# Kernel optimization log

Hardware: AMD Instinct MI355X
Metric: run time of the kernel (lower is better)

## Reference

```python
import jax, jax.numpy as jnp
import numpy as np

N = 8192        # total mesh nodes
M1 = 6000       # nodes set from x (full 3D coords)
M2 = 2000       # nodes set from y (coords 0 and 2 only)
B = 4           # batch
K = 4           # smoothing steps


def setup_inputs() -> dict:
    key = jax.random.key(0)
    k1, k2, k3, k4 = jax.random.split(key, 4)
    # Sparse-ish random symmetric-flavored adjacency, stored dense (as the module does).
    A = (jax.random.uniform(k1, (N, N)) < 0.002).astype(jnp.float32)
    idx = jnp.arange(N)
    # Ring edges guarantee every row has degree >= 1 (avoid divide-by-zero).
    A = A.at[idx, (idx + 1) % N].set(1.0)
    A = A.at[(idx + 1) % N, idx].set(1.0)
    # Diagonal: 1 for first half, 0 for second half -> output mask selects N//2 nodes.
    A = A.at[idx, idx].set((idx < N // 2).astype(jnp.float32))
    # Disjoint index sets for the scatter writes.
    perm = jax.random.permutation(k2, N)
    li1 = perm[:M1].astype(jnp.int64)
    li2 = perm[M1:M1 + M2].astype(jnp.int64)
    x = jax.random.normal(k3, (B, M1 * 3), dtype=jnp.float32)
    y = jax.random.normal(k4, (B, M2 * 2), dtype=jnp.float32)
    temp_zero = jnp.zeros((N, 3), dtype=jnp.float32)
    return {"x": x, "y": y, "edge_matrix": A, "temp_zero": temp_zero,
            "local_indices_1": li1, "local_indices_2": li2, "k": K}


def reference(x, y, edge_matrix, temp_zero, local_indices_1, local_indices_2, k):
    b = x.shape[0]
    # Scatter-build the graph state [B, N, 3].
    temp = jnp.broadcast_to(temp_zero[None], (b,) + temp_zero.shape)
    temp = temp.at[:, local_indices_1, :].set(x.reshape(b, -1, 3))
    y2 = y.reshape(b, -1, 2)
    temp = temp.at[:, local_indices_2, 0].set(y2[:, :, 0])
    temp = temp.at[:, local_indices_2, 2].set(y2[:, :, 1])
    # Degree normalization vector (row sums), computed once.
    deg = jnp.sum(edge_matrix, axis=1)  # [N]
    mesh = temp
    for _ in range(k):
        # smoother: (mesh^T @ A^T)^T == A @ mesh over the node dim, then /degree.
        mesh = jnp.einsum('ij,bjc->bic', edge_matrix, mesh) / deg[None, :, None]
    # Gather rows whose diagonal adjacency entry is zero.
    mask = jnp.diag(edge_matrix) == 0
    return mesh[:, mask, :]
```

## Files before the change

### kernel.cpp

```cpp
#include <hip/hip_runtime.h>

#define NN   8192
#define NN3  (NN * 3)
#define ST   16
#define CAP  64
#define M1   6000
#define M2   2000
#define SENT NN
#define CT   256
#define SB   64
#define NPS  (NN / SB)

typedef unsigned short u16;
typedef float f4v __attribute__((ext_vector_type(4)));

__global__ __launch_bounds__(256) void build_ell(const float* __restrict__ A,
                                                 u16* __restrict__ cols,
                                                 int* __restrict__ nch,
                                                 float* __restrict__ rdeg,
                                                 const int* __restrict__ li1,
                                                 const int* __restrict__ li2,
                                                 const float* __restrict__ x,
                                                 const float* __restrict__ y,
                                                 float* __restrict__ mesh_a,
                                                 float* __restrict__ mesh_b,
                                                 int B) {
    const int tid = threadIdx.x;
    __shared__ u16 enc16[NN];
    __shared__ int cnt;

    if (blockIdx.x >= NN) {
        const int sid = blockIdx.x - NN;
        for (int i = tid; i < NN; i += 256) enc16[i] = 0;
        __syncthreads();
        for (int j = tid; j < M1; j += 256) enc16[li1[j]] = (u16)(1 + j);
        for (int j = tid; j < M2; j += 256) enc16[li2[j]] = (u16)(M1 + 1 + j);
        __syncthreads();
        if (sid == 0 && tid < ST) {
            mesh_a[NN * ST + tid] = 0.f;
            mesh_b[NN * ST + tid] = 0.f;
        }
        const int lo = sid * NPS;
        for (int t = tid; t < NPS * ST; t += 256) {
            const int il = t >> 4, q = t & 15;
            const int i = lo + il;
            float v = 0.f;
            if (q < 12) {
                const u16 e = enc16[i];
                if (e) {
                    const int b = q / 3, c = q - b * 3;
                    if (e <= M1)      v = x[(b * M1 + (e - 1)) * 3 + c];
                    else if (c != 1)  v = y[(b * M2 + (e - (M1 + 1))) * 2 + (c >> 1)];
                }
            }
            mesh_a[(size_t)i * ST + q] = v;
        }
        return;
    }

    const int row = blockIdx.x;
    if (tid == 0) cnt = 0;
    __syncthreads();
    const f4v* __restrict__ Arow = (const f4v*)(A + (size_t)row * NN);
    f4v v[8];
    #pragma unroll
    for (int k = 0; k < 8; ++k)
        v[k] = __builtin_nontemporal_load(&Arow[k * 256 + tid]);
    u16* __restrict__ crow = cols + row * CAP;
    #pragma unroll
    for (int k = 0; k < 8; ++k) {
        const int base = (k * 256 + tid) * 4;
        if (v[k].x != 0.f) { int p = atomicAdd(&cnt, 1); if (p < CAP) crow[p] = (u16)(base);     }
        if (v[k].y != 0.f) { int p = atomicAdd(&cnt, 1); if (p < CAP) crow[p] = (u16)(base + 1); }
        if (v[k].z != 0.f) { int p = atomicAdd(&cnt, 1); if (p < CAP) crow[p] = (u16)(base + 2); }
        if (v[k].w != 0.f) { int p = atomicAdd(&cnt, 1); if (p < CAP) crow[p] = (u16)(base + 3); }
    }
    __syncthreads();
    int c = cnt;
    if (c > CAP) c = CAP;
    const int padded = (c + 7) & ~7;
    if (tid < padded - c && c + tid < CAP) crow[c + tid] = (u16)SENT;
    if (tid == 0) {
        nch[row]  = padded >> 3;
        rdeg[row] = 1.0f / (float)cnt;
    }
}

#define GATHER8(mb)                                                             \
    { const uint4 q = cr[ch];                                                   \
      acc += mb[(q.x & 0xFFFF) * ST + bc] + mb[(q.x >> 16) * ST + bc]           \
           + mb[(q.y & 0xFFFF) * ST + bc] + mb[(q.y >> 16) * ST + bc]           \
           + mb[(q.z & 0xFFFF) * ST + bc] + mb[(q.z >> 16) * ST + bc]           \
           + mb[(q.w & 0xFFFF) * ST + bc] + mb[(q.w >> 16) * ST + bc]; }

__global__ __launch_bounds__(CT) void spmv_full(const u16* __restrict__ cols,
                                                const int* __restrict__ nch,
                                                const float* __restrict__ rdeg,
                                                const float* __restrict__ src,
                                                float* __restrict__ dst) {
    const int g = blockIdx.x * CT + threadIdx.x;
    const int i = g / 12, bc = g - (g / 12) * 12;
    const int n = nch[i];
    const float rd = rdeg[i];
    const uint4* __restrict__ cr = (const uint4*)(cols + i * CAP);
    const float* __restrict__ mb = src;
    float acc = 0.f;
    for (int ch = 0; ch < n; ++ch) GATHER8(mb);
    dst[(size_t)i * ST + bc] = acc * rd;
}

__global__ __launch_bounds__(CT) void spmv_last(const u16* __restrict__ cols,
                                                const int* __restrict__ nch,
                                                const float* __restrict__ rdeg,
                                                const float* __restrict__ src,
                                                float* __restrict__ out) {
    const int g = blockIdx.x * CT + threadIdx.x;
    const int i2 = g / 12, bc = g - (g / 12) * 12;
    const int b = bc / 3, c = bc - b * 3;
    const int i = NN / 2 + i2;
    const int n = nch[i];
    const float rd = rdeg[i];
    const uint4* __restrict__ cr = (const uint4*)(cols + i * CAP);
    const float* __restrict__ mb = src;
    float acc = 0.f;
    for (int ch = 0; ch < n; ++ch) GATHER8(mb);
    out[((size_t)b * (NN / 2) + i2) * 3 + c] = acc * rd;
}

extern "C" void kernel_launch(void* const* d_in, const int* in_sizes, int n_in,
                              void* d_out, int out_size, void* d_ws, size_t ws_size,
                              hipStream_t stream) {
    const float* x   = (const float*)d_in[0];
    const float* y   = (const float*)d_in[1];
    const float* A   = (const float*)d_in[2];
    const int*   li1 = (const int*)d_in[4];
    const int*   li2 = (const int*)d_in[5];

    const int B = in_sizes[0] / (M1 * 3);

    char* ws = (char*)d_ws;
    u16*   cols   = (u16*)ws;    ws += (size_t)NN * CAP * 2;
    int*   nchv   = (int*)ws;    ws += (size_t)NN * 4;
    float* rdeg   = (float*)ws;  ws += (size_t)NN * 4;
    float* mesh_a = (float*)ws;  ws += (size_t)(NN + 1) * ST * 4;
    float* mesh_b = (float*)ws;

    build_ell<<<NN + SB, 256, 0, stream>>>(A, cols, nchv, rdeg,
                                           li1, li2, x, y, mesh_a, mesh_b, B);

    const int nbf = NN * 12 / CT;
    spmv_full<<<nbf, CT, 0, stream>>>(cols, nchv, rdeg, mesh_a, mesh_b);
    spmv_full<<<nbf, CT, 0, stream>>>(cols, nchv, rdeg, mesh_b, mesh_a);
    spmv_full<<<nbf, CT, 0, stream>>>(cols, nchv, rdeg, mesh_a, mesh_b);

    const int nbl = (NN / 2) * 12 / CT;
    spmv_last<<<nbl, CT, 0, stream>>>(cols, nchv, rdeg, mesh_b, (float*)d_out);
}
```

Before: 63.55 us.

## Fuse first smoothing step into ELL build kernel, drop one SpMV launch

Each row block now builds the scatter index table in shared memory and computes the first smoothing step directly from its nonzero columns, writing the normalized result into mesh_a. This removes one full SpMV kernel launch and the separate mesh initialization blocks. In exchange, every one of the row blocks redundantly rebuilds the node-index table, reading the index arrays and doing thousands of shared-memory scatters per block.

```diff
diff --git a/kernel.cpp b/kernel.cpp
--- a/kernel.cpp
+++ b/kernel.cpp
@@ -1,88 +1,86 @@
 #include <hip/hip_runtime.h>
 
 #define NN   8192
-#define NN3  (NN * 3)
 #define ST   16
 #define CAP  64
 #define M1   6000
 #define M2   2000
 #define SENT NN
 #define CT   256
-#define SB   64
-#define NPS  (NN / SB)
 
 typedef unsigned short u16;
 typedef float f4v __attribute__((ext_vector_type(4)));
 
-__global__ __launch_bounds__(256) void build_ell(const float* __restrict__ A,
-                                                 u16* __restrict__ cols,
-                                                 int* __restrict__ nch,
-                                                 float* __restrict__ rdeg,
-                                                 const int* __restrict__ li1,
-                                                 const int* __restrict__ li2,
-                                                 const float* __restrict__ x,
-                                                 const float* __restrict__ y,
-                                                 float* __restrict__ mesh_a,
-                                                 float* __restrict__ mesh_b,
-                                                 int B) {
+__global__ __launch_bounds__(256) void build_fused(
+    const float* __restrict__ A,
+    u16* __restrict__ cols, int* __restrict__ nch, float* __restrict__ rdeg,
+    const int* __restrict__ li1, const int* __restrict__ li2,
+    const float* __restrict__ x, const float* __restrict__ y,
+    float* __restrict__ mesh_a, float* __restrict__ mesh_b)
+{
+    const int row = blockIdx.x;
     const int tid = threadIdx.x;
-    __shared__ u16 enc16[NN];
-    __shared__ int cnt;
+    __shared__ u16  enc16[NN];
+    __shared__ u16  scol[CAP];
+    __shared__ float sacc[12];
+    __shared__ int  cnt;
 
-    if (blockIdx.x >= NN) {
-        const int sid = blockIdx.x - NN;
-        for (int i = tid; i < NN; i += 256) enc16[i] = 0;
-        __syncthreads();
-        for (int j = tid; j < M1; j += 256) enc16[li1[j]] = (u16)(1 + j);
-        for (int j = tid; j < M2; j += 256) enc16[li2[j]] = (u16)(M1 + 1 + j);
-        __syncthreads();
-        if (sid == 0 && tid < ST) {
-            mesh_a[NN * ST + tid] = 0.f;
-            mesh_b[NN * ST + tid] = 0.f;
-        }
-        const int lo = sid * NPS;
-        for (int t = tid; t < NPS * ST; t += 256) {
-            const int il = t >> 4, q = t & 15;
-            const int i = lo + il;
-            float v = 0.f;
-            if (q < 12) {
-                const u16 e = enc16[i];
-                if (e) {
-                    const int b = q / 3, c = q - b * 3;
-                    if (e <= M1)      v = x[(b * M1 + (e - 1)) * 3 + c];
-                    else if (c != 1)  v = y[(b * M2 + (e - (M1 + 1))) * 2 + (c >> 1)];
-                }
-            }
-            mesh_a[(size_t)i * ST + q] = v;
-        }
-        return;
-    }
-
-    const int row = blockIdx.x;
-    if (tid == 0) cnt = 0;
-    __syncthreads();
     const f4v* __restrict__ Arow = (const f4v*)(A + (size_t)row * NN);
     f4v v[8];
     #pragma unroll
     for (int k = 0; k < 8; ++k)
         v[k] = __builtin_nontemporal_load(&Arow[k * 256 + tid]);
+
+    {
+        unsigned int* e32 = (unsigned int*)enc16;
+        #pragma unroll
+        for (int t = 0; t < 16; ++t) e32[t * 256 + tid] = 0u;
+    }
+    if (tid < 12) sacc[tid] = 0.f;
+    if (tid == 0) cnt = 0;
+    __syncthreads();
+    for (int j = tid; j < M1; j += 256) enc16[li1[j]] = (u16)(1 + j);
+    for (int j = tid; j < M2; j += 256) enc16[li2[j]] = (u16)(M1 + 1 + j);
+    __syncthreads();
+
     u16* __restrict__ crow = cols + row * CAP;
     #pragma unroll
     for (int k = 0; k < 8; ++k) {
         const int base = (k * 256 + tid) * 4;
-        if (v[k].x != 0.f) { int p = atomicAdd(&cnt, 1); if (p < CAP) crow[p] = (u16)(base);     }
-        if (v[k].y != 0.f) { int p = atomicAdd(&cnt, 1); if (p < CAP) crow[p] = (u16)(base + 1); }
-        if (v[k].z != 0.f) { int p = atomicAdd(&cnt, 1); if (p < CAP) crow[p] = (u16)(base + 2); }
-        if (v[k].w != 0.f) { int p = atomicAdd(&cnt, 1); if (p < CAP) crow[p] = (u16)(base + 3); }
+        #pragma unroll
+        for (int e4 = 0; e4 < 4; ++e4) {
+            if (v[k][e4] != 0.f) {
+                const int col = base + e4;
+                const int p = atomicAdd(&cnt, 1);
+                if (p < CAP) { crow[p] = (u16)col; scol[p] = (u16)col; }
+            }
+        }
     }
     __syncthreads();
-    int c = cnt;
-    if (c > CAP) c = CAP;
-    const int padded = (c + 7) & ~7;
-    if (tid < padded - c && c + tid < CAP) crow[c + tid] = (u16)SENT;
-    if (tid == 0) {
-        nch[row]  = padded >> 3;
-        rdeg[row] = 1.0f / (float)cnt;
+
+    const int cc = (cnt > CAP) ? CAP : cnt;
+    for (int t = tid; t < cc * 12; t += 256) {
+        const int nz = t / 12, q = t - nz * 12;
+        const u16 e = enc16[scol[nz]];
+        float val = 0.f;
+        if (e) {
+            const int b = q / 3, c = q - b * 3;
+            if (e <= (u16)M1)  val = x[(b * M1 + (e - 1)) * 3 + c];
+            else if (c != 1)   val = y[(b * M2 + (e - (M1 + 1))) * 2 + (c >> 1)];
+        }
+        if (val != 0.f) atomicAdd(&sacc[q], val);
+    }
+
+    const int padded = (cc + 7) & ~7;
+    if (tid < padded - cc && cc + tid < CAP) crow[cc + tid] = (u16)SENT;
+    __syncthreads();
+
+    const float rd = 1.0f / (float)cnt;
+    if (tid == 0) { nch[row] = padded >> 3; rdeg[row] = rd; }
+    if (tid < 12) mesh_a[(size_t)row * ST + tid] = sacc[tid] * rd;
+    if (row == 0 && tid >= 32 && tid < 48) {
+        mesh_a[(size_t)NN * ST + (tid - 32)] = 0.f;
+        mesh_b[(size_t)NN * ST + (tid - 32)] = 0.f;
     }
 }
 
@@ -136,8 +134,6 @@
     const int*   li1 = (const int*)d_in[4];
     const int*   li2 = (const int*)d_in[5];
 
-    const int B = in_sizes[0] / (M1 * 3);
-
     char* ws = (char*)d_ws;
     u16*   cols   = (u16*)ws;    ws += (size_t)NN * CAP * 2;
     int*   nchv   = (int*)ws;    ws += (size_t)NN * 4;
@@ -145,14 +141,13 @@
     float* mesh_a = (float*)ws;  ws += (size_t)(NN + 1) * ST * 4;
     float* mesh_b = (float*)ws;
 
-    build_ell<<<NN + SB, 256, 0, stream>>>(A, cols, nchv, rdeg,
-                                           li1, li2, x, y, mesh_a, mesh_b, B);
+    build_fused<<<NN, 256, 0, stream>>>(A, cols, nchv, rdeg,
+                                        li1, li2, x, y, mesh_a, mesh_b);
 
     const int nbf = NN * 12 / CT;
     spmv_full<<<nbf, CT, 0, stream>>>(cols, nchv, rdeg, mesh_a, mesh_b);
     spmv_full<<<nbf, CT, 0, stream>>>(cols, nchv, rdeg, mesh_b, mesh_a);
-    spmv_full<<<nbf, CT, 0, stream>>>(cols, nchv, rdeg, mesh_a, mesh_b);
 
     const int nbl = (NN / 2) * 12 / CT;
-    spmv_last<<<nbl, CT, 0, stream>>>(cols, nchv, rdeg, mesh_b, (float*)d_out);
+    spmv_last<<<nbl, CT, 0, stream>>>(cols, nchv, rdeg, mesh_a, (float*)d_out);
 }
```

Measured after the change: 77.32 us. 21.7% more time.
